# Kernel tuning notes

Measured on AMD Instinct MI355X. Metric: run time of the kernel, lower is better.

The kernel has to match this reference:

```python
import jax, jax.numpy as jnp
import numpy as np

IN_DIM = 64
OUT_DIM = 64
NUM_SPLINES = 8
DEGREE = 3
EPS = 1e-8


def setup_inputs() -> dict:
    key = jax.random.key(0)
    k1, k2 = jax.random.split(key, 2)
    x = jax.random.normal(k1, (4, 512, IN_DIM), dtype=jnp.float32)
    control_points = jax.random.normal(k2, (OUT_DIM, IN_DIM, NUM_SPLINES), dtype=jnp.float32) * 0.1
    K = NUM_SPLINES + DEGREE + 1  # 12 knots
    knots = jnp.broadcast_to(jnp.linspace(-1.0, 1.0, K, dtype=jnp.float32), (OUT_DIM, IN_DIM, K)).copy()
    activation_weights = jnp.ones((OUT_DIM, IN_DIM, 4), dtype=jnp.float32) / 4.0
    return {"x": x, "control_points": control_points, "knots": knots, "activation_weights": activation_weights}


def _bspline_basis(x, knots, degree):
    # x: (b, n, d); knots: (O, d, K) -> basis (b, O, n, d, K-degree-1)
    xs = x[:, None, :, :, None]          # (b, 1, n, d, 1)
    t = knots[None, :, None, :, :]       # (1, O, 1, d, K)
    # Cox-de Boor degree 0: indicator of half-open knot interval
    B = ((xs >= t[..., :-1]) & (xs < t[..., 1:])).astype(x.dtype)  # (b, O, n, d, K-1)
    for k in range(1, degree + 1):
        Km = B.shape[-1]
        c1 = (xs - t[..., : Km - 1]) / (t[..., k : k + Km - 1] - t[..., : Km - 1] + EPS)
        c2 = (t[..., k + 1 : k + Km] - xs) / (t[..., k + 1 : k + Km] - t[..., 1:Km] + EPS)
        B = c1 * B[..., :-1] + c2 * B[..., 1:]
    return B


def reference(x, control_points, knots, activation_weights):
    # B-spline branch: (b,O,n,d,S) x (O,d,S) -> (b,O,n)
    basis = _bspline_basis(x, knots, DEGREE)
    out = jnp.einsum('bonds,ods->bon', basis, control_points)
    # activation-mixture branch: activations are independent of the out dim
    acts = jnp.stack([jax.nn.relu(x), jnp.tanh(x), jax.nn.sigmoid(x), x], axis=-1)  # (b,n,d,4)
    act_out = jnp.einsum('bnda,oda->bon', acts, activation_weights)
    return out + 0.1 * act_out  # (b, out_dim, n)
```

## Files before the change

kernel.cpp:

```cpp
#include <hip/hip_runtime.h>

#define D_IN 64
#define D_OUT 64
#define NS 8
#define NK 12
#define NF 12
#define NBN 2048
#define KSPLIT 8
#define DCH 8
#define KCH (DCH * NF)
#define BNT 64
#define NT (NBN / BNT)
#define KAN_EPS 1e-8f

__device__ int g_cnt[NT];

__device__ inline float rcp_(float a) { return __builtin_amdgcn_rcpf(a); }

__device__ inline void basis8(float xv, const float* __restrict__ t, float* __restrict__ B)
{
    float Bb[11];
    #pragma unroll
    for (int i = 0; i < 11; ++i) Bb[i] = (xv >= t[i] && xv < t[i + 1]) ? 1.f : 0.f;
    #pragma unroll
    for (int i = 0; i < 10; ++i)
        Bb[i] = (xv - t[i]) * rcp_(t[i + 1] - t[i] + KAN_EPS) * Bb[i]
              + (t[i + 2] - xv) * rcp_(t[i + 2] - t[i + 1] + KAN_EPS) * Bb[i + 1];
    #pragma unroll
    for (int i = 0; i < 9; ++i)
        Bb[i] = (xv - t[i]) * rcp_(t[i + 2] - t[i] + KAN_EPS) * Bb[i]
              + (t[i + 3] - xv) * rcp_(t[i + 3] - t[i + 1] + KAN_EPS) * Bb[i + 1];
    #pragma unroll
    for (int i = 0; i < 8; ++i)
        Bb[i] = (xv - t[i]) * rcp_(t[i + 3] - t[i] + KAN_EPS) * Bb[i]
              + (t[i + 4] - xv) * rcp_(t[i + 4] - t[i + 1] + KAN_EPS) * Bb[i + 1];
    #pragma unroll
    for (int i = 0; i < 8; ++i) B[i] = Bb[i];
}

__global__ __launch_bounds__(512)
void kan_fused(const float* __restrict__ x,
               const float* __restrict__ cp,
               const float* __restrict__ knots,
               const float* __restrict__ aw,
               float* __restrict__ partial,
               float* __restrict__ out)
{
    __shared__ float sF[KCH][BNT];
    __shared__ float sW[KCH][D_OUT];
    __shared__ int s_mism, s_last;

    const int bt   = blockIdx.x;
    const int ks   = blockIdx.y;
    const int tid  = threadIdx.x;
    const int lane = tid & 63;
    const int wv   = __builtin_amdgcn_readfirstlane(tid >> 6);
    const int d0   = ks * DCH;
    const int bn   = bt * BNT + lane;

    if (tid == 0) { s_mism = 0; }
    __syncthreads();

    {
        const int d = d0 + wv;
        const float xv = x[bn * D_IN + d];
        float t[NK];
        #pragma unroll
        for (int j = 0; j < NK; ++j) t[j] = knots[d * NK + j];
        float B[8];
        basis8(xv, t, B);
        #pragma unroll
        for (int s = 0; s < 8; ++s) sF[wv * NF + s][lane] = B[s];
        const float v = __expf(-xv);
        sF[wv * NF + 8][lane]  = fmaxf(xv, 0.f);
        sF[wv * NF + 9][lane]  = 2.f * rcp_(1.f + v * v) - 1.f;
        sF[wv * NF + 10][lane] = rcp_(1.f + v);
        sF[wv * NF + 11][lane] = xv;
    }

    {
        const int dg = tid >> 6;
        const int o  = lane;
        const int d  = d0 + dg;
        const int od = o * D_IN + d;
        const float4 c0 = *(const float4*)&cp[od * NS];
        const float4 c1 = *(const float4*)&cp[od * NS + 4];
        const float4 av = *(const float4*)&aw[od * 4];
        sW[dg * NF + 0][o] = c0.x;  sW[dg * NF + 1][o] = c0.y;
        sW[dg * NF + 2][o] = c0.z;  sW[dg * NF + 3][o] = c0.w;
        sW[dg * NF + 4][o] = c1.x;  sW[dg * NF + 5][o] = c1.y;
        sW[dg * NF + 6][o] = c1.z;  sW[dg * NF + 7][o] = c1.w;
        sW[dg * NF + 8][o]  = 0.1f * av.x;
        sW[dg * NF + 9][o]  = 0.1f * av.y;
        sW[dg * NF + 10][o] = 0.1f * av.z;
        sW[dg * NF + 11][o] = 0.1f * av.w;

        int m = 0;
        #pragma unroll
        for (int j = 0; j < NK; ++j)
            m |= (knots[od * NK + j] != knots[d * NK + j]) ? 1 : 0;
        if (m) atomicOr(&s_mism, 1);
    }
    __syncthreads();

    const int og8 = __builtin_amdgcn_readfirstlane(wv * 8);
    float acc[8] = {0.f, 0.f, 0.f, 0.f, 0.f, 0.f, 0.f, 0.f};

    if (s_mism == 0) {
        #pragma unroll 4
        for (int k = 0; k < KCH; ++k) {
            const float f   = sF[k][lane];
            const float4 wA = *(const float4*)&sW[k][og8];
            const float4 wB = *(const float4*)&sW[k][og8 + 4];
            acc[0] = fmaf(f, wA.x, acc[0]);  acc[1] = fmaf(f, wA.y, acc[1]);
            acc[2] = fmaf(f, wA.z, acc[2]);  acc[3] = fmaf(f, wA.w, acc[3]);
            acc[4] = fmaf(f, wB.x, acc[4]);  acc[5] = fmaf(f, wB.y, acc[5]);
            acc[6] = fmaf(f, wB.z, acc[6]);  acc[7] = fmaf(f, wB.w, acc[7]);
        }
    } else {
        for (int dg = 0; dg < DCH; ++dg) {
            const int d = d0 + dg;
            const float xv = x[bn * D_IN + d];
            const float v  = __expf(-xv);
            const float Ra = rcp_(1.f + v * v), Rb = rcp_(1.f + v);
            const float fr = fmaxf(xv, 0.f), fth = 2.f * Ra - 1.f;
            for (int j = 0; j < 8; ++j) {
                const int o  = og8 + j;
                const int od = o * D_IN + d;
                float t2[NK];
                #pragma unroll
                for (int jj = 0; jj < NK; ++jj) t2[jj] = knots[od * NK + jj];
                float B[8];
                basis8(xv, t2, B);
                float sp = 0.f;
                #pragma unroll
                for (int s = 0; s < NS; ++s) sp += B[s] * cp[od * NS + s];
                sp += 0.1f * (aw[od * 4 + 0] * fr + aw[od * 4 + 1] * fth
                            + aw[od * 4 + 2] * Rb + aw[od * 4 + 3] * xv);
                acc[j] += sp;
            }
        }
    }

    #pragma unroll
    for (int j = 0; j < 8; ++j)
        partial[(size_t)(ks * D_OUT + og8 + j) * NBN + bn] = acc[j];

    __syncthreads();
    if (tid == 0) {
        __threadfence();
        s_last = (atomicAdd(&g_cnt[bt], 1) == KSPLIT - 1);
    }
    __syncthreads();
    if (!s_last) return;

    if (tid == 0) g_cnt[bt] = 0;
    __threadfence();
    #pragma unroll
    for (int j = 0; j < 8; ++j) {
        float s = 0.f;
        #pragma unroll
        for (int q = 0; q < KSPLIT; ++q)
            s += partial[(size_t)(q * D_OUT + og8 + j) * NBN + bn];
        const int b = bn >> 9;
        const int n = bn & 511;
        out[((b * D_OUT + og8 + j) << 9) | n] = s;
    }
}

extern "C" void kernel_launch(void* const* d_in, const int* in_sizes, int n_in,
                              void* d_out, int out_size, void* d_ws, size_t ws_size,
                              hipStream_t stream) {
    const float* x     = (const float*)d_in[0];
    const float* cp    = (const float*)d_in[1];
    const float* knots = (const float*)d_in[2];
    const float* aw    = (const float*)d_in[3];
    float* out     = (float*)d_out;
    float* partial = (float*)d_ws;

    dim3 grid(NT, KSPLIT);
    kan_fused<<<grid, 512, 0, stream>>>(x, cp, knots, aw, partial, out);
}
```

Baseline: 25.46 us.

## Use 4x4 register tiling with 256-thread blocks and float4 partial stores

Blocks shrink from 512 to 256 threads. Each thread now computes a 4x4 tile of outputs by batch position, reading float4 from both the feature and weight shared arrays. This replaces the 8-output-per-lane scheme, which needed one scalar plus two float4 LDS reads per k. Partial-sum stores and the final reduction are vectorized to float4. The cost is that each thread does two loops of basis and weight staging, and each block has half as many waves to hide latency.

```diff
diff --git a/kernel.cpp b/kernel.cpp
--- a/kernel.cpp
+++ b/kernel.cpp
@@ -38,7 +38,7 @@
     for (int i = 0; i < 8; ++i) B[i] = Bb[i];
 }
 
-__global__ __launch_bounds__(512)
+__global__ __launch_bounds__(256)
 void kan_fused(const float* __restrict__ x,
                const float* __restrict__ cp,
                const float* __restrict__ knots,
@@ -50,37 +50,40 @@
     __shared__ float sW[KCH][D_OUT];
     __shared__ int s_mism, s_last;
 
-    const int bt   = blockIdx.x;
-    const int ks   = blockIdx.y;
-    const int tid  = threadIdx.x;
-    const int lane = tid & 63;
-    const int wv   = __builtin_amdgcn_readfirstlane(tid >> 6);
-    const int d0   = ks * DCH;
-    const int bn   = bt * BNT + lane;
-
-    if (tid == 0) { s_mism = 0; }
-    __syncthreads();
-
-    {
-        const int d = d0 + wv;
-        const float xv = x[bn * D_IN + d];
+    const int bt  = blockIdx.x;
+    const int ks  = blockIdx.y;
+    const int tid = threadIdx.x;
+    const int d0  = ks * DCH;
+
+    if (tid == 0) s_mism = 0;
+    __syncthreads();
+
+    #pragma unroll
+    for (int rep = 0; rep < 2; ++rep) {
+        const int p    = tid + rep * 256;
+        const int dg   = p >> 6;
+        const int lane = p & 63;
+        const int d    = d0 + dg;
+        const float xv = x[(bt * BNT + lane) * D_IN + d];
         float t[NK];
         #pragma unroll
         for (int j = 0; j < NK; ++j) t[j] = knots[d * NK + j];
         float B[8];
         basis8(xv, t, B);
         #pragma unroll
-        for (int s = 0; s < 8; ++s) sF[wv * NF + s][lane] = B[s];
+        for (int s = 0; s < 8; ++s) sF[dg * NF + s][lane] = B[s];
         const float v = __expf(-xv);
-        sF[wv * NF + 8][lane]  = fmaxf(xv, 0.f);
-        sF[wv * NF + 9][lane]  = 2.f * rcp_(1.f + v * v) - 1.f;
-        sF[wv * NF + 10][lane] = rcp_(1.f + v);
-        sF[wv * NF + 11][lane] = xv;
-    }
-
-    {
-        const int dg = tid >> 6;
-        const int o  = lane;
+        sF[dg * NF + 8][lane]  = fmaxf(xv, 0.f);
+        sF[dg * NF + 9][lane]  = 2.f * rcp_(1.f + v * v) - 1.f;
+        sF[dg * NF + 10][lane] = rcp_(1.f + v);
+        sF[dg * NF + 11][lane] = xv;
+    }
+
+    #pragma unroll
+    for (int rep = 0; rep < 2; ++rep) {
+        const int q  = tid + rep * 256;
+        const int o  = q & 63;
+        const int dg = q >> 6;
         const int d  = d0 + dg;
         const int od = o * D_IN + d;
         const float4 c0 = *(const float4*)&cp[od * NS];
@@ -103,48 +106,64 @@
     }
     __syncthreads();
 
-    const int og8 = __builtin_amdgcn_readfirstlane(wv * 8);
-    float acc[8] = {0.f, 0.f, 0.f, 0.f, 0.f, 0.f, 0.f, 0.f};
+    const int og4 = (tid >> 4) << 2;
+    const int bnq = (tid & 15) << 2;
+    float acc[4][4] = {};
 
     if (s_mism == 0) {
-        #pragma unroll 4
+        #pragma unroll 8
         for (int k = 0; k < KCH; ++k) {
-            const float f   = sF[k][lane];
-            const float4 wA = *(const float4*)&sW[k][og8];
-            const float4 wB = *(const float4*)&sW[k][og8 + 4];
-            acc[0] = fmaf(f, wA.x, acc[0]);  acc[1] = fmaf(f, wA.y, acc[1]);
-            acc[2] = fmaf(f, wA.z, acc[2]);  acc[3] = fmaf(f, wA.w, acc[3]);
-            acc[4] = fmaf(f, wB.x, acc[4]);  acc[5] = fmaf(f, wB.y, acc[5]);
-            acc[6] = fmaf(f, wB.z, acc[6]);  acc[7] = fmaf(f, wB.w, acc[7]);
+            const float4 f4 = *(const float4*)&sF[k][bnq];
+            const float4 w4 = *(const float4*)&sW[k][og4];
+            acc[0][0] = fmaf(w4.x, f4.x, acc[0][0]);
+            acc[0][1] = fmaf(w4.x, f4.y, acc[0][1]);
+            acc[0][2] = fmaf(w4.x, f4.z, acc[0][2]);
+            acc[0][3] = fmaf(w4.x, f4.w, acc[0][3]);
+            acc[1][0] = fmaf(w4.y, f4.x, acc[1][0]);
+            acc[1][1] = fmaf(w4.y, f4.y, acc[1][1]);
+            acc[1][2] = fmaf(w4.y, f4.z, acc[1][2]);
+            acc[1][3] = fmaf(w4.y, f4.w, acc[1][3]);
+            acc[2][0] = fmaf(w4.z, f4.x, acc[2][0]);
+            acc[2][1] = fmaf(w4.z, f4.y, acc[2][1]);
+            acc[2][2] = fmaf(w4.z, f4.z, acc[2][2]);
+            acc[2][3] = fmaf(w4.z, f4.w, acc[2][3]);
+            acc[3][0] = fmaf(w4.w, f4.x, acc[3][0]);
+            acc[3][1] = fmaf(w4.w, f4.y, acc[3][1]);
+            acc[3][2] = fmaf(w4.w, f4.z, acc[3][2]);
+            acc[3][3] = fmaf(w4.w, f4.w, acc[3][3]);
         }
     } else {
         for (int dg = 0; dg < DCH; ++dg) {
             const int d = d0 + dg;
-            const float xv = x[bn * D_IN + d];
-            const float v  = __expf(-xv);
-            const float Ra = rcp_(1.f + v * v), Rb = rcp_(1.f + v);
-            const float fr = fmaxf(xv, 0.f), fth = 2.f * Ra - 1.f;
-            for (int j = 0; j < 8; ++j) {
-                const int o  = og8 + j;
-                const int od = o * D_IN + d;
-                float t2[NK];
-                #pragma unroll
-                for (int jj = 0; jj < NK; ++jj) t2[jj] = knots[od * NK + jj];
-                float B[8];
-                basis8(xv, t2, B);
-                float sp = 0.f;
-                #pragma unroll
-                for (int s = 0; s < NS; ++s) sp += B[s] * cp[od * NS + s];
-                sp += 0.1f * (aw[od * 4 + 0] * fr + aw[od * 4 + 1] * fth
-                            + aw[od * 4 + 2] * Rb + aw[od * 4 + 3] * xv);
-                acc[j] += sp;
+            #pragma unroll
+            for (int bi = 0; bi < 4; ++bi) {
+                const float xv = x[(bt * BNT + bnq + bi) * D_IN + d];
+                const float v  = __expf(-xv);
+                const float Ra = rcp_(1.f + v * v), Rb = rcp_(1.f + v);
+                const float fr = fmaxf(xv, 0.f), fth = 2.f * Ra - 1.f;
+                for (int oi = 0; oi < 4; ++oi) {
+                    const int od = (og4 + oi) * D_IN + d;
+                    float t2[NK];
+                    #pragma unroll
+                    for (int jj = 0; jj < NK; ++jj) t2[jj] = knots[od * NK + jj];
+                    float B[8];
+                    basis8(xv, t2, B);
+                    float sp = 0.f;
+                    #pragma unroll
+                    for (int s = 0; s < NS; ++s) sp += B[s] * cp[od * NS + s];
+                    sp += 0.1f * (aw[od * 4 + 0] * fr + aw[od * 4 + 1] * fth
+                                + aw[od * 4 + 2] * Rb + aw[od * 4 + 3] * xv);
+                    acc[oi][bi] += sp;
+                }
             }
         }
     }
 
-    #pragma unroll
-    for (int j = 0; j < 8; ++j)
-        partial[(size_t)(ks * D_OUT + og8 + j) * NBN + bn] = acc[j];
+    const int bnbase = bt * BNT + bnq;
+    #pragma unroll
+    for (int j = 0; j < 4; ++j)
+        *(float4*)&partial[(size_t)(ks * D_OUT + og4 + j) * NBN + bnbase] =
+            make_float4(acc[j][0], acc[j][1], acc[j][2], acc[j][3]);
 
     __syncthreads();
     if (tid == 0) {
@@ -157,14 +176,16 @@
     if (tid == 0) g_cnt[bt] = 0;
     __threadfence();
     #pragma unroll
-    for (int j = 0; j < 8; ++j) {
-        float s = 0.f;
-        #pragma unroll
-        for (int q = 0; q < KSPLIT; ++q)
-            s += partial[(size_t)(q * D_OUT + og8 + j) * NBN + bn];
-        const int b = bn >> 9;
-        const int n = bn & 511;
-        out[((b * D_OUT + og8 + j) << 9) | n] = s;
+    for (int j = 0; j < 4; ++j) {
+        float4 s = make_float4(0.f, 0.f, 0.f, 0.f);
+        #pragma unroll
+        for (int q = 0; q < KSPLIT; ++q) {
+            const float4 p = *(const float4*)&partial[(size_t)(q * D_OUT + og4 + j) * NBN + bnbase];
+            s.x += p.x; s.y += p.y; s.z += p.z; s.w += p.w;
+        }
+        const int b = bnbase >> 9;
+        const int n = bnbase & 511;
+        *(float4*)&out[((b * D_OUT + og4 + j) << 9) + n] = s;
     }
 }
 
@@ -179,5 +200,5 @@
     float* partial = (float*)d_ws;
 
     dim3 grid(NT, KSPLIT);
-    kan_fused<<<grid, 512, 0, stream>>>(x, cp, knots, aw, partial, out);
+    kan_fused<<<grid, 256, 0, stream>>>(x, cp, knots, aw, partial, out);
 }
```

After: 24.66 us. 3.1% less time.
